# Kernel tuning notes

Measured on AMD Instinct MI355X. Metric: run time of the kernel, lower is better.

The kernel has to match this reference:

```python
import jax, jax.numpy as jnp
import numpy as np

N, C, D = 8192, 1000, 128


def setup_inputs() -> dict:
    key = jax.random.key(0)
    kx, kp = jax.random.split(key)
    x = jax.random.normal(kx, (N, D), dtype=jnp.float32)
    # Matches torch.randn(1, features_dim) per class, concatenated -> (C, D)
    prototypes = jax.random.normal(kp, (C, D), dtype=jnp.float32)
    return {"x": x, "prototypes": prototypes}


def reference(x, prototypes):
    # x: (N, D), prototypes: (C, D)
    # Faithful to: d = sum((x[:,None,:] - P[None,:,:])**2, axis=2); logits = -d
    diff = x[:, None, :] - prototypes[None, :, :]  # (N, C, D), fused by XLA
    d = jnp.sum(diff * diff, axis=2)               # (N, C)
    return -d
```

## Files before the change

### kernel.cpp

```cpp
#include <hip/hip_runtime.h>
#include <hip/hip_bf16.h>

typedef __attribute__((ext_vector_type(8))) short short8_t;
typedef __attribute__((ext_vector_type(4))) float f32x4;

static __device__ __forceinline__ unsigned short f2bf(float f) {
    unsigned int u = __float_as_uint(f);
    unsigned int r = u + 0x7fffu + ((u >> 16) & 1u);
    return (unsigned short)(r >> 16);
}

__global__ __launch_bounds__(256) void prep_kernel(
        const float* __restrict__ src, unsigned short* __restrict__ dst,
        float* __restrict__ sq, int rows_valid, int rows_total) {
    int t = threadIdx.x;
    int row = blockIdx.x * 8 + (t >> 5);
    int lane32 = t & 31;
    if (row >= rows_total) return;
    float4 v = make_float4(0.f, 0.f, 0.f, 0.f);
    if (row < rows_valid)
        v = reinterpret_cast<const float4*>(src + (size_t)row * 128)[lane32];
    ushort4 b;
    b.x = f2bf(v.x); b.y = f2bf(v.y); b.z = f2bf(v.z); b.w = f2bf(v.w);
    reinterpret_cast<ushort4*>(dst + (size_t)row * 128)[lane32] = b;
    float s = v.x*v.x + v.y*v.y + v.z*v.z + v.w*v.w;
    #pragma unroll
    for (int m = 16; m >= 1; m >>= 1) s += __shfl_xor(s, m, 64);
    if (lane32 == 0) sq[row] = s;
}

#define LDT 136

__global__ __launch_bounds__(512) void main_kernel(
        const float* __restrict__ X,
        const unsigned short* __restrict__ Bw,
        const float* __restrict__ psq,
        float* __restrict__ out) {
    __shared__ unsigned short As[32][LDT];
    __shared__ unsigned short Bs[2][128][LDT];
    __shared__ float xq_s[32];
    __shared__ float trans[8][16][16];

    const int t = threadIdx.x;
    const int slab0 = blockIdx.x * 32;

    {
        int r = t >> 4;
        int c8 = (t & 15) * 8;
        const float4* src = reinterpret_cast<const float4*>(X + (size_t)(slab0 + r) * 128 + c8);
        float4 v0 = src[0], v1 = src[1];
        short8_t b;
        b[0] = (short)f2bf(v0.x); b[1] = (short)f2bf(v0.y);
        b[2] = (short)f2bf(v0.z); b[3] = (short)f2bf(v0.w);
        b[4] = (short)f2bf(v1.x); b[5] = (short)f2bf(v1.y);
        b[6] = (short)f2bf(v1.z); b[7] = (short)f2bf(v1.w);
        *reinterpret_cast<short8_t*>(&As[r][c8]) = b;
        float s = v0.x*v0.x + v0.y*v0.y + v0.z*v0.z + v0.w*v0.w
                + v1.x*v1.x + v1.y*v1.y + v1.z*v1.z + v1.w*v1.w;
        s += __shfl_xor(s, 1, 64);
        s += __shfl_xor(s, 2, 64);
        s += __shfl_xor(s, 4, 64);
        s += __shfl_xor(s, 8, 64);
        if ((t & 15) == 0) xq_s[r] = s;
    }
    {
        int r = t >> 2;
        int cb = (t & 3) * 32;
        const unsigned short* src = Bw + (size_t)r * 128 + cb;
        #pragma unroll
        for (int k = 0; k < 4; ++k) {
            short8_t v = *reinterpret_cast<const short8_t*>(src + k * 8);
            *reinterpret_cast<short8_t*>(&Bs[0][r][cb + k * 8]) = v;
        }
    }
    __syncthreads();

    const int wave = t >> 6;
    const int lane = t & 63;
    const int wm  = (wave >> 2) * 16;
    const int wcb = (wave & 3) * 32;
    const int lr  = lane & 15;
    const int lkb = (lane >> 4) * 8;

    short8_t afrag[4];
    #pragma unroll
    for (int ks = 0; ks < 4; ++ks)
        afrag[ks] = *reinterpret_cast<const short8_t*>(&As[wm + lr][ks * 32 + lkb]);
    const float4 xq4 = *reinterpret_cast<const float4*>(&xq_s[wm + (lane >> 4) * 4]);

    const int rr = lane >> 2;
    const int cq = (lane & 3) * 4;
    const int rbase = (lane >> 4) * 4;

    int cur = 0;
    #pragma unroll 1
    for (int cn = 0; cn < 8; ++cn) {
        short8_t pf[4];
        if (cn < 7) {
            int r = t >> 2;
            int cb = (t & 3) * 32;
            const unsigned short* src = Bw + (size_t)((cn + 1) * 128 + r) * 128 + cb;
            #pragma unroll
            for (int k = 0; k < 4; ++k)
                pf[k] = *reinterpret_cast<const short8_t*>(src + k * 8);
        }
        #pragma unroll
        for (int ni = 0; ni < 2; ++ni) {
            f32x4 acc = {0.f, 0.f, 0.f, 0.f};
            #pragma unroll
            for (int ks = 0; ks < 4; ++ks) {
                short8_t bfrag = *reinterpret_cast<const short8_t*>(
                        &Bs[cur][wcb + ni * 16 + lr][ks * 32 + lkb]);
                acc = __builtin_amdgcn_mfma_f32_16x16x32_bf16(afrag[ks], bfrag, acc, 0, 0, 0);
            }
            #pragma unroll
            for (int j = 0; j < 4; ++j)
                trans[wave][rbase + j][lr] = 2.f * acc[j] - ((const float*)&xq4)[j];
            float4 tv = *reinterpret_cast<const float4*>(&trans[wave][rr][cq]);
            int col = cn * 128 + wcb + ni * 16 + cq;
            if (col < 1000) {
                float4 pq = *reinterpret_cast<const float4*>(psq + col);
                tv.x -= pq.x; tv.y -= pq.y; tv.z -= pq.z; tv.w -= pq.w;
                *reinterpret_cast<float4*>(out + (size_t)(slab0 + wm + rr) * 1000 + col) = tv;
            }
        }
        if (cn < 7) {
            int r = t >> 2;
            int cb = (t & 3) * 32;
            #pragma unroll
            for (int k = 0; k < 4; ++k)
                *reinterpret_cast<short8_t*>(&Bs[cur ^ 1][r][cb + k * 8]) = pf[k];
            __syncthreads();
            cur ^= 1;
        }
    }
}

__global__ __launch_bounds__(256) void naive_kernel(
        const float* __restrict__ x, const float* __restrict__ p,
        float* __restrict__ out) {
    long long idx = (long long)blockIdx.x * 256 + threadIdx.x;
    if (idx >= (long long)8192 * 1000) return;
    int n = (int)(idx / 1000);
    int c = (int)(idx % 1000);
    const float4* xr = reinterpret_cast<const float4*>(x + (size_t)n * 128);
    const float4* pr = reinterpret_cast<const float4*>(p + (size_t)c * 128);
    float d = 0.f;
    #pragma unroll
    for (int i = 0; i < 32; ++i) {
        float4 a = xr[i], b = pr[i];
        float dx = a.x - b.x, dy = a.y - b.y, dz = a.z - b.z, dw = a.w - b.w;
        d += dx * dx + dy * dy + dz * dz + dw * dw;
    }
    out[idx] = -d;
}

extern "C" void kernel_launch(void* const* d_in, const int* in_sizes, int n_in,
                              void* d_out, int out_size, void* d_ws, size_t ws_size,
                              hipStream_t stream) {
    const float* x = (const float*)d_in[0];
    const float* p = (const float*)d_in[1];
    float* out = (float*)d_out;

    const size_t pb_elems = (size_t)1024 * 128;
    const size_t need = pb_elems * 2 + 1024 * 4;

    if (ws_size >= need) {
        unsigned short* pb = (unsigned short*)d_ws;
        float* psq = (float*)(pb + pb_elems);
        prep_kernel<<<128, 256, 0, stream>>>(p, pb, psq, 1000, 1024);
        main_kernel<<<256, 512, 0, stream>>>(x, pb, psq, out);
    } else {
        naive_kernel<<<((size_t)8192 * 1000 + 255) / 256, 256, 0, stream>>>(x, p, out);
    }
}
```

Before: 24.43 us.

## Stage full output slab in LDS and write rows contiguously

Each block now writes its whole 32x1000 result tile into a swizzled LDS buffer (aliased with the A tile) and then streams complete rows to global memory with wide coalesced stores. The per-wave transpose-through-LDS scratch is removed. B is processed in 64-column chunks with a single buffer and two barriers per step instead of a double buffer. The goal is to replace scattered 16-byte partial-row stores with full-row streaming writes. The cost is about 129 KB of dynamic LDS per block, which limits occupancy to one block per CU, plus an extra host attribute call on every launch.

After: 28.14 us. 15.2% more time.

```diff
diff --git a/kernel.cpp b/kernel.cpp
--- a/kernel.cpp
+++ b/kernel.cpp
@@ -29,17 +29,19 @@
     if (lane32 == 0) sq[row] = s;
 }
 
-#define LDT 136
+#define LDB 132
+#define OSTRIDE 1008
 
 __global__ __launch_bounds__(512) void main_kernel(
         const float* __restrict__ X,
         const unsigned short* __restrict__ Bw,
         const float* __restrict__ psq,
         float* __restrict__ out) {
-    __shared__ unsigned short As[32][LDT];
-    __shared__ unsigned short Bs[2][128][LDT];
+    extern __shared__ float dynlds[];
+    unsigned short (*As)[LDB] = reinterpret_cast<unsigned short(*)[LDB]>(dynlds);
+    float* out_s = dynlds;
+    __shared__ unsigned short Bs[64][LDB];
     __shared__ float xq_s[32];
-    __shared__ float trans[8][16][16];
 
     const int t = threadIdx.x;
     const int slab0 = blockIdx.x * 32;
@@ -64,74 +66,81 @@
         if ((t & 15) == 0) xq_s[r] = s;
     }
     {
-        int r = t >> 2;
-        int cb = (t & 3) * 32;
-        const unsigned short* src = Bw + (size_t)r * 128 + cb;
-        #pragma unroll
-        for (int k = 0; k < 4; ++k) {
-            short8_t v = *reinterpret_cast<const short8_t*>(src + k * 8);
-            *reinterpret_cast<short8_t*>(&Bs[0][r][cb + k * 8]) = v;
-        }
+        int r = t >> 3;
+        int c = (t & 7) * 16;
+        const unsigned short* src = Bw + (size_t)r * 128 + c;
+        *reinterpret_cast<short8_t*>(&Bs[r][c])     = *reinterpret_cast<const short8_t*>(src);
+        *reinterpret_cast<short8_t*>(&Bs[r][c + 8]) = *reinterpret_cast<const short8_t*>(src + 8);
     }
     __syncthreads();
 
-    const int wave = t >> 6;
-    const int lane = t & 63;
-    const int wm  = (wave >> 2) * 16;
-    const int wcb = (wave & 3) * 32;
-    const int lr  = lane & 15;
-    const int lkb = (lane >> 4) * 8;
+    const int wave  = t >> 6;
+    const int lane  = t & 63;
+    const int wm    = (wave >> 2) * 16;
+    const int wn    = (wave & 3) * 16;
+    const int lr    = lane & 15;
+    const int lkb   = (lane >> 4) * 8;
+    const int rbase = (lane >> 4) * 4;
 
     short8_t afrag[4];
     #pragma unroll
     for (int ks = 0; ks < 4; ++ks)
         afrag[ks] = *reinterpret_cast<const short8_t*>(&As[wm + lr][ks * 32 + lkb]);
-    const float4 xq4 = *reinterpret_cast<const float4*>(&xq_s[wm + (lane >> 4) * 4]);
+    __syncthreads();
 
-    const int rr = lane >> 2;
-    const int cq = (lane & 3) * 4;
-    const int rbase = (lane >> 4) * 4;
-
-    int cur = 0;
     #pragma unroll 1
-    for (int cn = 0; cn < 8; ++cn) {
-        short8_t pf[4];
-        if (cn < 7) {
-            int r = t >> 2;
-            int cb = (t & 3) * 32;
-            const unsigned short* src = Bw + (size_t)((cn + 1) * 128 + r) * 128 + cb;
+    for (int cn = 0; cn < 16; ++cn) {
+        short8_t pf0, pf1;
+        if (cn < 15) {
+            int r = t >> 3, c = (t & 7) * 16;
+            const unsigned short* src = Bw + (size_t)((cn + 1) * 64 + r) * 128 + c;
+            pf0 = *reinterpret_cast<const short8_t*>(src);
+            pf1 = *reinterpret_cast<const short8_t*>(src + 8);
+        }
+        f32x4 acc = {0.f, 0.f, 0.f, 0.f};
+        #pragma unroll
+        for (int ks = 0; ks < 4; ++ks) {
+            short8_t bfrag = *reinterpret_cast<const short8_t*>(
+                    &Bs[wn + lr][ks * 32 + lkb]);
+            acc = __builtin_amdgcn_mfma_f32_16x16x32_bf16(afrag[ks], bfrag, acc, 0, 0, 0);
+        }
+        int col = cn * 64 + wn + lr;
+        if (col < 1000) {
+            float pq = psq[col];
             #pragma unroll
-            for (int k = 0; k < 4; ++k)
-                pf[k] = *reinterpret_cast<const short8_t*>(src + k * 8);
-        }
-        #pragma unroll
-        for (int ni = 0; ni < 2; ++ni) {
-            f32x4 acc = {0.f, 0.f, 0.f, 0.f};
-            #pragma unroll
-            for (int ks = 0; ks < 4; ++ks) {
-                short8_t bfrag = *reinterpret_cast<const short8_t*>(
-                        &Bs[cur][wcb + ni * 16 + lr][ks * 32 + lkb]);
-                acc = __builtin_amdgcn_mfma_f32_16x16x32_bf16(afrag[ks], bfrag, acc, 0, 0, 0);
-            }
-            #pragma unroll
-            for (int j = 0; j < 4; ++j)
-                trans[wave][rbase + j][lr] = 2.f * acc[j] - ((const float*)&xq4)[j];
-            float4 tv = *reinterpret_cast<const float4*>(&trans[wave][rr][cq]);
-            int col = cn * 128 + wcb + ni * 16 + cq;
-            if (col < 1000) {
-                float4 pq = *reinterpret_cast<const float4*>(psq + col);
-                tv.x -= pq.x; tv.y -= pq.y; tv.z -= pq.z; tv.w -= pq.w;
-                *reinterpret_cast<float4*>(out + (size_t)(slab0 + wm + rr) * 1000 + col) = tv;
+            for (int j = 0; j < 4; ++j) {
+                int row = wm + rbase + j;
+                int pc = col + ((row >> 2) & 3) * 8;
+                if (pc >= OSTRIDE) pc -= OSTRIDE;
+                out_s[row * OSTRIDE + pc] = 2.f * acc[j] - pq;
             }
         }
-        if (cn < 7) {
-            int r = t >> 2;
-            int cb = (t & 3) * 32;
-            #pragma unroll
-            for (int k = 0; k < 4; ++k)
-                *reinterpret_cast<short8_t*>(&Bs[cur ^ 1][r][cb + k * 8]) = pf[k];
+        if (cn < 15) {
             __syncthreads();
-            cur ^= 1;
+            int r = t >> 3, c = (t & 7) * 16;
+            *reinterpret_cast<short8_t*>(&Bs[r][c])     = pf0;
+            *reinterpret_cast<short8_t*>(&Bs[r][c + 8]) = pf1;
+            __syncthreads();
+        }
+    }
+    __syncthreads();
+
+    #pragma unroll
+    for (int ri = 0; ri < 4; ++ri) {
+        int r = wave * 4 + ri;
+        float xq = xq_s[r];
+        int sw = ((r >> 2) & 3) * 8;
+        size_t gbase = (size_t)(slab0 + r) * 1000;
+        #pragma unroll
+        for (int seg = 0; seg < 4; ++seg) {
+            int c = seg * 256 + lane * 4;
+            if (c < 1000) {
+                int pc = c + sw;
+                if (pc >= OSTRIDE) pc -= OSTRIDE;
+                f32x4 v = *reinterpret_cast<const f32x4*>(&out_s[r * OSTRIDE + pc]);
+                float4 o = make_float4(v[0] - xq, v[1] - xq, v[2] - xq, v[3] - xq);
+                *reinterpret_cast<float4*>(out + gbase + c) = o;
+            }
         }
     }
 }
@@ -164,12 +173,17 @@
 
     const size_t pb_elems = (size_t)1024 * 128;
     const size_t need = pb_elems * 2 + 1024 * 4;
+    const int dyn_bytes = 32 * OSTRIDE * 4;
 
-    if (ws_size >= need) {
+    hipError_t attr_ok = hipFuncSetAttribute(
+            (const void*)main_kernel,
+            hipFuncAttributeMaxDynamicSharedMemorySize, dyn_bytes);
+
+    if (ws_size >= need && attr_ok == hipSuccess) {
         unsigned short* pb = (unsigned short*)d_ws;
         float* psq = (float*)(pb + pb_elems);
         prep_kernel<<<128, 256, 0, stream>>>(p, pb, psq, 1000, 1024);
-        main_kernel<<<256, 512, 0, stream>>>(x, pb, psq, out);
+        main_kernel<<<256, 512, dyn_bytes, stream>>>(x, pb, psq, out);
     } else {
         naive_kernel<<<((size_t)8192 * 1000 + 255) / 256, 256, 0, stream>>>(x, p, out);
     }
```
